# Kernel tuning notes

Measured on AMD Instinct MI355X. Metric: run time of the kernel, lower is better.

The kernel has to match this reference:

```python
import jax, jax.numpy as jnp
import numpy as np

N = 50000   # nodes
E = 800000  # edges per timestep
T = 2
IN_C = 128
HID = 128


def gcn_conv(x, src, dst, W, b):
    """PyG GCNConv: add self-loops, symmetric normalization, linear, scatter-add, bias."""
    n = x.shape[0]
    loop = jnp.arange(n, dtype=src.dtype)
    s = jnp.concatenate([src, loop])  # [E+N]
    d = jnp.concatenate([dst, loop])
    h = x @ W                          # [N, H]
    deg = jax.ops.segment_sum(jnp.ones_like(d, dtype=x.dtype), d, num_segments=n)
    dinv = jnp.where(deg > 0, jax.lax.rsqrt(deg), 0.0)
    norm = dinv[s] * dinv[d]           # [E+N]
    msg = h[s] * norm[:, None]         # gather + scale
    out = jax.ops.segment_sum(msg, d, num_segments=n)  # scatter-add
    return out + b


def setup_inputs() -> dict:
    key = jax.random.key(0)
    ks = jax.random.split(key, 6)
    x_seq = jax.random.normal(ks[0], (T, N, IN_C), dtype=jnp.float32)
    edge_indices = jax.random.randint(ks[1], (T, 2, E), 0, N, dtype=jnp.int64)
    W1 = jax.random.normal(ks[2], (IN_C, HID), dtype=jnp.float32) * (1.0 / np.sqrt(IN_C))
    b1 = jnp.zeros((HID,), dtype=jnp.float32)
    W2 = jax.random.normal(ks[3], (HID, HID), dtype=jnp.float32) * (1.0 / np.sqrt(HID))
    b2 = jnp.zeros((HID,), dtype=jnp.float32)
    Wc = jax.random.normal(ks[4], (HID, 1), dtype=jnp.float32) * (1.0 / np.sqrt(HID))
    bc = jnp.zeros((1,), dtype=jnp.float32)
    return {"x_seq": x_seq, "edge_indices": edge_indices, "W1": W1, "b1": b1,
            "W2": W2, "b2": b2, "Wc": Wc, "bc": bc}


def reference(x_seq, edge_indices, W1, b1, W2, b2, Wc, bc):
    outputs = []
    for t in range(T):  # small fixed timestep loop, as in original
        x_t = x_seq[t]
        src = edge_indices[t, 0]
        dst = edge_indices[t, 1]
        h = jax.nn.relu(gcn_conv(x_t, src, dst, W1, b1))
        # dropout is inference-identity (eval mode)
        h = gcn_conv(h, src, dst, W2, b2)
        outputs.append(h)
    final = outputs[-1]
    importance_out = (final @ Wc + bc).squeeze(-1)  # [N]
    return (importance_out, *outputs)
```

## Files before the change

kernel.cpp:

```cpp
#include <hip/hip_runtime.h>
#include <hip/hip_bf16.h>

typedef unsigned int u32;
typedef unsigned short u16;
typedef unsigned long long u64;
typedef __bf16 bf16x8 __attribute__((ext_vector_type(8)));
typedef short short8 __attribute__((ext_vector_type(8)));
typedef float floatx4 __attribute__((ext_vector_type(4)));

__device__ inline float b2f(u16 b) { return __uint_as_float((u32)b << 16); }
__device__ inline float lo2f(u32 p) { return __uint_as_float(p << 16); }
__device__ inline float hi2f(u32 p) { return __uint_as_float(p & 0xffff0000u); }
__device__ inline u16 f2bs(float f) {
    __hip_bfloat16 h = __float2bfloat16(f);
    return *reinterpret_cast<u16*>(&h);
}
__device__ inline float ldext(const void* p, int fl, int i) {
    return fl ? ((const float*)p)[i] : b2f(((const u16*)p)[i]);
}

__global__ __launch_bounds__(64) void detect_kernel(const int* __restrict__ eb,
                                                    const u32* __restrict__ xw,
                                                    int* __restrict__ flags,
                                                    int S, int n) {
    __shared__ int sh[64 * 3];
    int lane = threadIdx.x & 63;
    int zc = 0, explo = 0;
#pragma unroll
    for (int r = 0; r < 4; ++r) {
        int i = 64 * r + lane;
        zc += (eb[2 * i + 1] == 0) ? 1 : 0;
        u32 w = xw[i];
        int e = (int)((w >> 7) & 0xFF);
        explo += (e >= 96 && e <= 140) ? 1 : 0;
    }
    sh[lane] = zc;
    sh[64 + lane] = explo;
    __syncthreads();
    int fl = 0;
    {
        int z = 0;
        for (int j = 0; j < 64; ++j) z += sh[j];
        fl = (z > 200) ? 1 : 0;
    }
    int vc = 0;
#pragma unroll
    for (int r = 0; r < 4; ++r) {
        int li = S / 2 + 64 * r + lane;
        int v = fl ? eb[2 * li] : eb[li];
        vc += ((unsigned)v < (unsigned)n) ? 1 : 0;
    }
    sh[128 + lane] = vc;
    __syncthreads();
    if (lane == 0) {
        int vtot = 0, etot = 0;
        for (int j = 0; j < 64; ++j) vtot += sh[128 + j];
        for (int j = 0; j < 64; ++j) etot += sh[64 + j];
        flags[0] = fl;
        flags[1] = (etot >= 192) ? 0 : 1;
        flags[2] = (vtot >= 240) ? (S / 4) : (S / 8);
    }
}

__device__ inline int load_edge(const int* eb, int fl, int idx) {
    return eb[fl ? (idx << 1) : idx];
}

#define PCHUNK 4096
__global__ __launch_bounds__(256) void part_kernel(const int* __restrict__ eb,
                                                   const int* __restrict__ flags,
                                                   int* __restrict__ bkcnt,
                                                   u64* __restrict__ pairs,
                                                   int n, int shift, int capP) {
    __shared__ int cnt[512];
    __shared__ int gbase[512];
    const int E = flags[2];
    const int fl = flags[0];
    const int nbuk = (2 * n + (1 << shift) - 1) >> shift;
    const int tid = threadIdx.x;
    for (int i = tid; i < nbuk; i += 256) cnt[i] = 0;
    __syncthreads();
    const int e0 = blockIdx.x * PCHUNK;
    u32 sv[16]; int gv[16], rk[16];
#pragma unroll
    for (int j = 0; j < 16; ++j) {
        int e = e0 + j * 256 + tid;
        u32 gs = 0; int g = -1;
        if (e < 2 * E) {
            int t = (e >= E) ? 1 : 0;
            int le = e - t * E;
            gs = (u32)(t * n) + (u32)load_edge(eb, fl, t * 2 * E + le);
            unsigned du = (unsigned)load_edge(eb, fl, t * 2 * E + E + le);
            if (du < (unsigned)n) g = t * n + (int)du;
        }
        sv[j] = gs;
        gv[j] = g;
        rk[j] = (g >= 0) ? atomicAdd(&cnt[g >> shift], 1) : 0;
    }
    __syncthreads();
    for (int b = tid; b < nbuk; b += 256) {
        int c = cnt[b];
        gbase[b] = c ? atomicAdd(&bkcnt[b], c) : 0;
    }
    __syncthreads();
#pragma unroll
    for (int j = 0; j < 16; ++j) {
        if (gv[j] >= 0) {
            int b = gv[j] >> shift;
            int idx = gbase[b] + rk[j];
            if (idx < capP)
                pairs[(size_t)b * capP + idx] =
                    ((u64)(u32)gv[j] << 32) | sv[j];
        }
    }
}

__global__ __launch_bounds__(256) void scat_kernel(const u64* __restrict__ pairs,
                                                   const int* __restrict__ bkcnt,
                                                   int* __restrict__ deg,
                                                   int* __restrict__ off,
                                                   float* __restrict__ dinv,
                                                   int* __restrict__ ssrc,
                                                   int n2, int shift, int capP) {
    __shared__ int hist[1024];
    __shared__ int lscan[256];
    const int b = blockIdx.x;
    const int d0 = b << shift;
    if (d0 >= n2) return;
    int nn = (1 << shift);
    if (d0 + nn > n2) nn = n2 - d0;
    const int tid = threadIdx.x;
    for (int j = tid; j < nn; j += 256) hist[j] = 0;
    __syncthreads();
    int cnt = bkcnt[b];
    if (cnt > capP) cnt = capP;
    const int gb = b * capP;
    const u64* pb = pairs + (size_t)gb;
    for (int i = tid; i < cnt; i += 256) {
        unsigned dl = (unsigned)(int)(pb[i] >> 32) - (unsigned)d0;
        if (dl < (unsigned)nn) atomicAdd(&hist[dl], 1);
    }
    __syncthreads();
    int base4 = tid * 4;
    int s0 = 0, s1 = 0, s2 = 0, s3 = 0;
    if (base4 < nn) {
        s0 = hist[base4];
        s1 = (base4 + 1 < nn) ? hist[base4 + 1] : 0;
        s2 = (base4 + 2 < nn) ? hist[base4 + 2] : 0;
        s3 = (base4 + 3 < nn) ? hist[base4 + 3] : 0;
    }
    int p0 = (s0 + 3) & ~3, p1 = (s1 + 3) & ~3;
    int p2 = (s2 + 3) & ~3, p3 = (s3 + 3) & ~3;
    int tsum = p0 + p1 + p2 + p3;
    lscan[tid] = tsum;
    __syncthreads();
    int val = tsum;
    for (int o = 1; o < 256; o <<= 1) {
        int add = (tid >= o) ? lscan[tid - o] : 0;
        __syncthreads();
        val += add;
        lscan[tid] = val;
        __syncthreads();
    }
    int texcl = val - tsum;
    if (base4 < nn) {
        int g = d0 + base4;
        int o0 = gb + texcl;
        deg[g] = s0; off[g] = o0; dinv[g] = rsqrtf((float)(s0 + 1));
        hist[base4] = o0;
        if (base4 + 1 < nn) {
            int o1 = o0 + p0;
            deg[g + 1] = s1; off[g + 1] = o1; dinv[g + 1] = rsqrtf((float)(s1 + 1));
            hist[base4 + 1] = o1;
        }
        if (base4 + 2 < nn) {
            int o2 = o0 + p0 + p1;
            deg[g + 2] = s2; off[g + 2] = o2; dinv[g + 2] = rsqrtf((float)(s2 + 1));
            hist[base4 + 2] = o2;
        }
        if (base4 + 3 < nn) {
            int o3 = o0 + p0 + p1 + p2;
            deg[g + 3] = s3; off[g + 3] = o3; dinv[g + 3] = rsqrtf((float)(s3 + 1));
            hist[base4 + 3] = o3;
        }
    }
    __syncthreads();
    const int limit = gb + capP;
    for (int i = tid; i < cnt; i += 256) {
        u64 p = pb[i];
        unsigned dl = (unsigned)(int)(p >> 32) - (unsigned)d0;
        if (dl < (unsigned)nn) {
            int pos = atomicAdd(&hist[dl], 1);
            if (pos < limit) ssrc[pos] = (int)(u32)p;
        }
    }
}

__global__ __launch_bounds__(256) void prep_w(const void* __restrict__ W1,
                                              const void* __restrict__ W2,
                                              const int* __restrict__ flags,
                                              u16* __restrict__ W1t,
                                              u16* __restrict__ W2t) {
    int tid = blockIdx.x * 256 + threadIdx.x;
    if (tid < 2 * 128 * 128) {
        int which = tid >> 14;
        int r = tid & 16383;
        const void* W = which ? W2 : W1;
        u16* Wt = which ? W2t : W1t;
        int c = r >> 7, k = r & 127;
        Wt[c * 128 + k] = f2bs(ldext(W, flags[1], k * 128 + c));
    }
}

__global__ __launch_bounds__(256) void gemm_mfma(const void* __restrict__ Xv,
                                                 int x_ext,
                                                 const u16* __restrict__ Wt,
                                                 const int* __restrict__ flags,
                                                 const float* __restrict__ dinv,
                                                 u16* __restrict__ hs, int n) {
    __shared__ u16 Ws[128 * 136];
    {
        u32* wsu = (u32*)Ws;
        const u32* wtu = (const u32*)Wt;
        for (int i = threadIdx.x; i < 128 * 64; i += 256) {
            int c = i >> 6, kk = i & 63;
            wsu[c * 68 + kk] = wtu[i];
        }
    }
    __syncthreads();

    const int wave = threadIdx.x >> 6;
    const int lane = threadIdx.x & 63;
    const int m = lane & 15;
    const int quad = lane >> 4;
    const int node0 = blockIdx.x * 64 + wave * 16;
    if (node0 >= n) return;

    const int xf32 = x_ext ? flags[1] : 0;
    int va = node0 + m;
    if (va > n - 1) va = n - 1;

    floatx4 acc[8];
#pragma unroll
    for (int t = 0; t < 8; ++t) acc[t] = (floatx4){0.f, 0.f, 0.f, 0.f};

#pragma unroll
    for (int ks = 0; ks < 4; ++ks) {
        bf16x8 a;
        if (xf32) {
            const float* Xf = (const float*)Xv + (size_t)va * 128 + ks * 32 + quad * 8;
            float4 x0 = *(const float4*)Xf;
            float4 x1 = *(const float4*)(Xf + 4);
            short8 as;
            as[0] = (short)f2bs(x0.x); as[1] = (short)f2bs(x0.y);
            as[2] = (short)f2bs(x0.z); as[3] = (short)f2bs(x0.w);
            as[4] = (short)f2bs(x1.x); as[5] = (short)f2bs(x1.y);
            as[6] = (short)f2bs(x1.z); as[7] = (short)f2bs(x1.w);
            a = __builtin_bit_cast(bf16x8, as);
        } else {
            const u16* Xb = (const u16*)Xv + (size_t)va * 128 + ks * 32 + quad * 8;
            a = *(const bf16x8*)Xb;
        }
#pragma unroll
        for (int t = 0; t < 8; ++t) {
            const bf16x8 b = *(const bf16x8*)(Ws + (16 * t + m) * 136 + ks * 32 + quad * 8);
            acc[t] = __builtin_amdgcn_mfma_f32_16x16x32_bf16(a, b, acc[t], 0, 0, 0);
        }
    }

#pragma unroll
    for (int r = 0; r < 4; ++r) {
        int v = node0 + quad * 4 + r;
        if (v < n) {
            float dv = dinv[v];
#pragma unroll
            for (int t = 0; t < 8; ++t)
                hs[(size_t)v * 128 + 16 * t + m] = f2bs(acc[t][r] * dv);
        }
    }
}

__global__ __launch_bounds__(256) void gather_kernel(const u16* __restrict__ hs,
                                                     const int* __restrict__ off,
                                                     const int* __restrict__ deg,
                                                     const int* __restrict__ ssrc,
                                                     const float* __restrict__ dinv,
                                                     const void* __restrict__ bias,
                                                     const int* __restrict__ flags,
                                                     float* __restrict__ outf,
                                                     u16* __restrict__ outb,
                                                     const void* __restrict__ Wc,
                                                     const void* __restrict__ bc,
                                                     float* __restrict__ imp,
                                                     int n2, int half, int relu) {
    int w = (blockIdx.x * 256 + threadIdx.x) >> 6;
    int lane = threadIdx.x & 63;
    if (w >= n2) return;

    const u32* hsu = (const u32*)hs;
    const unsigned nm1 = (unsigned)(n2 - 1);
    const unsigned zrow = (unsigned)n2;

    u32 pself = hsu[(size_t)w * 64 + lane];
    float ax = lo2f(pself), ay = hi2f(pself);
    int i = __builtin_amdgcn_readfirstlane(off[w]);
    int end = i + __builtin_amdgcn_readfirstlane(deg[w]);

    float bx = 0.f, by = 0.f, cx = 0.f, cy = 0.f, dx = 0.f, dy = 0.f;

    for (; i + 16 <= end; i += 16) {
        int4 qa = *(const int4*)(ssrc + i);
        int4 qb = *(const int4*)(ssrc + i + 4);
        int4 qc = *(const int4*)(ssrc + i + 8);
        int4 qd = *(const int4*)(ssrc + i + 12);
        unsigned s0 = (unsigned)qa.x; if (s0 > nm1) s0 = zrow;
        unsigned s1 = (unsigned)qa.y; if (s1 > nm1) s1 = zrow;
        unsigned s2 = (unsigned)qa.z; if (s2 > nm1) s2 = zrow;
        unsigned s3 = (unsigned)qa.w; if (s3 > nm1) s3 = zrow;
        unsigned s4 = (unsigned)qb.x; if (s4 > nm1) s4 = zrow;
        unsigned s5 = (unsigned)qb.y; if (s5 > nm1) s5 = zrow;
        unsigned s6 = (unsigned)qb.z; if (s6 > nm1) s6 = zrow;
        unsigned s7 = (unsigned)qb.w; if (s7 > nm1) s7 = zrow;
        unsigned s8 = (unsigned)qc.x; if (s8 > nm1) s8 = zrow;
        unsigned s9 = (unsigned)qc.y; if (s9 > nm1) s9 = zrow;
        unsigned sa = (unsigned)qc.z; if (sa > nm1) sa = zrow;
        unsigned sb = (unsigned)qc.w; if (sb > nm1) sb = zrow;
        unsigned sc = (unsigned)qd.x; if (sc > nm1) sc = zrow;
        unsigned sd = (unsigned)qd.y; if (sd > nm1) sd = zrow;
        unsigned se = (unsigned)qd.z; if (se > nm1) se = zrow;
        unsigned sf = (unsigned)qd.w; if (sf > nm1) sf = zrow;
        u32 v0 = hsu[(size_t)s0 * 64 + lane];
        u32 v1 = hsu[(size_t)s1 * 64 + lane];
        u32 v2 = hsu[(size_t)s2 * 64 + lane];
        u32 v3 = hsu[(size_t)s3 * 64 + lane];
        u32 v4 = hsu[(size_t)s4 * 64 + lane];
        u32 v5 = hsu[(size_t)s5 * 64 + lane];
        u32 v6 = hsu[(size_t)s6 * 64 + lane];
        u32 v7 = hsu[(size_t)s7 * 64 + lane];
        u32 v8 = hsu[(size_t)s8 * 64 + lane];
        u32 v9 = hsu[(size_t)s9 * 64 + lane];
        u32 va = hsu[(size_t)sa * 64 + lane];
        u32 vb = hsu[(size_t)sb * 64 + lane];
        u32 vc = hsu[(size_t)sc * 64 + lane];
        u32 vd = hsu[(size_t)sd * 64 + lane];
        u32 ve = hsu[(size_t)se * 64 + lane];
        u32 vf = hsu[(size_t)sf * 64 + lane];
        ax += lo2f(v0); ay += hi2f(v0);
        bx += lo2f(v1); by += hi2f(v1);
        cx += lo2f(v2); cy += hi2f(v2);
        dx += lo2f(v3); dy += hi2f(v3);
        ax += lo2f(v4); ay += hi2f(v4);
        bx += lo2f(v5); by += hi2f(v5);
        cx += lo2f(v6); cy += hi2f(v6);
        dx += lo2f(v7); dy += hi2f(v7);
        ax += lo2f(v8); ay += hi2f(v8);
        bx += lo2f(v9); by += hi2f(v9);
        cx += lo2f(va); cy += hi2f(va);
        dx += lo2f(vb); dy += hi2f(vb);
        ax += lo2f(vc); ay += hi2f(vc);
        bx += lo2f(vd); by += hi2f(vd);
        cx += lo2f(ve); cy += hi2f(ve);
        dx += lo2f(vf); dy += hi2f(vf);
    }
    for (; i < end; i += 4) {
        int4 qa = *(const int4*)(ssrc + i);
        unsigned s0 = (unsigned)qa.x; if (s0 > nm1) s0 = zrow;
        unsigned s1 = (unsigned)qa.y; if (i + 1 >= end || s1 > nm1) s1 = zrow;
        unsigned s2 = (unsigned)qa.z; if (i + 2 >= end || s2 > nm1) s2 = zrow;
        unsigned s3 = (unsigned)qa.w; if (i + 3 >= end || s3 > nm1) s3 = zrow;
        u32 v0 = hsu[(size_t)s0 * 64 + lane];
        u32 v1 = hsu[(size_t)s1 * 64 + lane];
        u32 v2 = hsu[(size_t)s2 * 64 + lane];
        u32 v3 = hsu[(size_t)s3 * 64 + lane];
        ax += lo2f(v0); ay += hi2f(v0);
        bx += lo2f(v1); by += hi2f(v1);
        cx += lo2f(v2); cy += hi2f(v2);
        dx += lo2f(v3); dy += hi2f(v3);
    }
    ax += bx + cx + dx;
    ay += by + cy + dy;

    int ffl = flags[1];
    float dv = dinv[w];
    float o0 = dv * ax + ldext(bias, ffl, 2 * lane);
    float o1 = dv * ay + ldext(bias, ffl, 2 * lane + 1);
    if (relu) {
        o0 = fmaxf(o0, 0.f);
        o1 = fmaxf(o1, 0.f);
    }
    if (outf) ((float2*)outf)[(size_t)w * 64 + lane] = make_float2(o0, o1);
    else ((u32*)outb)[(size_t)w * 64 + lane] = (u32)f2bs(o0) | ((u32)f2bs(o1) << 16);

    if (imp && w >= half) {
        float cb = o0 * ldext(Wc, ffl, 2 * lane) + o1 * ldext(Wc, ffl, 2 * lane + 1);
        cb += __shfl_xor(cb, 32);
        cb += __shfl_xor(cb, 16);
        cb += __shfl_xor(cb, 8);
        cb += __shfl_xor(cb, 4);
        cb += __shfl_xor(cb, 2);
        cb += __shfl_xor(cb, 1);
        if (lane == 0) imp[w - half] = cb + ldext(bc, ffl, 0);
    }
}

extern "C" void kernel_launch(void* const* d_in, const int* in_sizes, int n_in,
                              void* d_out, int out_size, void* d_ws, size_t ws_size,
                              hipStream_t stream) {
    const int T = 2, C = 128;
    const int N = in_sizes[0] / (T * C);
    const int S = in_sizes[1];
    const int Emax = S / 4;
    const int N2 = 2 * N;

    const void* x_seq = d_in[0];
    const int* edges = (const int*)d_in[1];
    const void* W1 = d_in[2];
    const void* b1 = d_in[3];
    const void* W2 = d_in[4];
    const void* b2 = d_in[5];
    const void* Wc = d_in[6];
    const void* bc = d_in[7];

    float* out = (float*)d_out;
    float* R = out + N;

    char* p = (char*)d_ws;
    auto alloc = [&](size_t bytes) {
        char* r = p;
        p += (bytes + 255) & ~(size_t)255;
        return r;
    };
    int* flags = (int*)alloc(256);
    int* deg = (int*)alloc((size_t)N2 * 4);
    int* off = (int*)alloc((size_t)N2 * 4);
    float* dinv = (float*)alloc((size_t)N2 * 4);
    int* bkcnt = (int*)alloc(512 * 4);

    int shift = 8;
    while ((((N2 + (1 << shift) - 1) >> shift) > 512) && shift < 10) ++shift;
    const int NBUK = (N2 + (1 << shift) - 1) >> shift;
    const size_t aliasBytes = (size_t)2 * N2 * C * 2;
    const int capP = (int)(aliasBytes / (8 * (size_t)NBUK)) & ~3;

    int* ssrc = (int*)alloc(((size_t)NBUK * capP + 256) * 4);
    u16* W1t = (u16*)alloc(128 * 128 * 2);
    u16* W2t = (u16*)alloc(128 * 128 * 2);
    u16* hsb = (u16*)alloc((size_t)(N2 + 2) * C * 2);
    u16* hmb = (u16*)alloc((size_t)N2 * C * 2);
    u64* pairs = (u64*)hsb;

    const int gP = (2 * Emax + PCHUNK - 1) / PCHUNK;
    const int gN2 = (N2 + 3) / 4;
    const int gG2 = (N2 + 63) / 64;
    const int gW = (2 * 128 * 128 + 255) / 256;

    detect_kernel<<<1, 64, 0, stream>>>(edges, (const u32*)x_seq, flags, S, N);
    prep_w<<<gW, 256, 0, stream>>>(W1, W2, flags, W1t, W2t);

    hipMemsetAsync(bkcnt, 0, 512 * 4, stream);
    part_kernel<<<gP, 256, 0, stream>>>(edges, flags, bkcnt, pairs, N, shift, capP);
    scat_kernel<<<NBUK, 256, 0, stream>>>(pairs, bkcnt, deg, off, dinv,
                                          ssrc, N2, shift, capP);
    hipMemsetAsync(hsb + (size_t)N2 * C, 0, C * 2, stream);

    gemm_mfma<<<gG2, 256, 0, stream>>>(x_seq, 1, W1t, flags, dinv, hsb, N2);
    gather_kernel<<<gN2, 256, 0, stream>>>(hsb, off, deg, ssrc, dinv, b1, flags,
                                           (float*)nullptr, hmb,
                                           nullptr, nullptr, (float*)nullptr,
                                           N2, N, 1);

    gemm_mfma<<<gG2, 256, 0, stream>>>(hmb, 0, W2t, flags, dinv, hsb, N2);
    gather_kernel<<<gN2, 256, 0, stream>>>(hsb, off, deg, ssrc, dinv, b2, flags,
                                           R, (u16*)nullptr,
                                           Wc, bc, out,
                                           N2, N, 0);
}
```

Before: 291.5 us.

## Fold memsets and weight prep into other kernels; persistent grid-stride gather

Zeroing of the bucket counters moves into detect_kernel and zeroing of the padding row moves into gemm_mfma, which removes two memset calls. The weight transpose is appended as extra blocks of part_kernel, removing the separate prep_w launch. The gather kernel becomes a persistent grid-stride loop over 2048 blocks that prefetches the next node's offset and degree and hoists the bias loads out of the loop. The aim is to cut launch and tail overhead, at the cost of less parallelism per node and some ordering risk for the padding row write.

```diff
diff --git a/kernel.cpp b/kernel.cpp
--- a/kernel.cpp
+++ b/kernel.cpp
@@ -22,9 +22,11 @@
 __global__ __launch_bounds__(64) void detect_kernel(const int* __restrict__ eb,
                                                     const u32* __restrict__ xw,
                                                     int* __restrict__ flags,
+                                                    int* __restrict__ bkcnt,
                                                     int S, int n) {
     __shared__ int sh[64 * 3];
     int lane = threadIdx.x & 63;
+    for (int j = lane; j < 512; j += 64) bkcnt[j] = 0;
     int zc = 0, explo = 0;
 #pragma unroll
     for (int r = 0; r < 4; ++r) {
@@ -71,9 +73,26 @@
                                                    const int* __restrict__ flags,
                                                    int* __restrict__ bkcnt,
                                                    u64* __restrict__ pairs,
-                                                   int n, int shift, int capP) {
+                                                   int n, int shift, int capP,
+                                                   int gP,
+                                                   const void* __restrict__ W1,
+                                                   const void* __restrict__ W2,
+                                                   u16* __restrict__ W1t,
+                                                   u16* __restrict__ W2t) {
     __shared__ int cnt[512];
     __shared__ int gbase[512];
+    if ((int)blockIdx.x >= gP) {
+        int tid = (blockIdx.x - gP) * 256 + threadIdx.x;
+        if (tid < 2 * 128 * 128) {
+            int which = tid >> 14;
+            int r = tid & 16383;
+            const void* W = which ? W2 : W1;
+            u16* Wt = which ? W2t : W1t;
+            int c = r >> 7, k = r & 127;
+            Wt[c * 128 + k] = f2bs(ldext(W, flags[1], k * 128 + c));
+        }
+        return;
+    }
     const int E = flags[2];
     const int fl = flags[0];
     const int nbuk = (2 * n + (1 << shift) - 1) >> shift;
@@ -196,28 +215,14 @@
     }
 }
 
-__global__ __launch_bounds__(256) void prep_w(const void* __restrict__ W1,
-                                              const void* __restrict__ W2,
-                                              const int* __restrict__ flags,
-                                              u16* __restrict__ W1t,
-                                              u16* __restrict__ W2t) {
-    int tid = blockIdx.x * 256 + threadIdx.x;
-    if (tid < 2 * 128 * 128) {
-        int which = tid >> 14;
-        int r = tid & 16383;
-        const void* W = which ? W2 : W1;
-        u16* Wt = which ? W2t : W1t;
-        int c = r >> 7, k = r & 127;
-        Wt[c * 128 + k] = f2bs(ldext(W, flags[1], k * 128 + c));
-    }
-}
-
 __global__ __launch_bounds__(256) void gemm_mfma(const void* __restrict__ Xv,
                                                  int x_ext,
                                                  const u16* __restrict__ Wt,
                                                  const int* __restrict__ flags,
                                                  const float* __restrict__ dinv,
                                                  u16* __restrict__ hs, int n) {
+    if (blockIdx.x == 0 && threadIdx.x < 64)
+        ((u32*)hs)[(size_t)n * 64 + threadIdx.x] = 0;
     __shared__ u16 Ws[128 * 136];
     {
         u32* wsu = (u32*)Ws;
@@ -292,114 +297,130 @@
                                                      const void* __restrict__ Wc,
                                                      const void* __restrict__ bc,
                                                      float* __restrict__ imp,
-                                                     int n2, int half, int relu) {
+                                                     int n2, int half, int relu,
+                                                     int nwaves) {
+    const int lane = threadIdx.x & 63;
     int w = (blockIdx.x * 256 + threadIdx.x) >> 6;
-    int lane = threadIdx.x & 63;
     if (w >= n2) return;
 
     const u32* hsu = (const u32*)hs;
     const unsigned nm1 = (unsigned)(n2 - 1);
     const unsigned zrow = (unsigned)n2;
-
-    u32 pself = hsu[(size_t)w * 64 + lane];
-    float ax = lo2f(pself), ay = hi2f(pself);
-    int i = __builtin_amdgcn_readfirstlane(off[w]);
-    int end = i + __builtin_amdgcn_readfirstlane(deg[w]);
-
-    float bx = 0.f, by = 0.f, cx = 0.f, cy = 0.f, dx = 0.f, dy = 0.f;
-
-    for (; i + 16 <= end; i += 16) {
-        int4 qa = *(const int4*)(ssrc + i);
-        int4 qb = *(const int4*)(ssrc + i + 4);
-        int4 qc = *(const int4*)(ssrc + i + 8);
-        int4 qd = *(const int4*)(ssrc + i + 12);
-        unsigned s0 = (unsigned)qa.x; if (s0 > nm1) s0 = zrow;
-        unsigned s1 = (unsigned)qa.y; if (s1 > nm1) s1 = zrow;
-        unsigned s2 = (unsigned)qa.z; if (s2 > nm1) s2 = zrow;
-        unsigned s3 = (unsigned)qa.w; if (s3 > nm1) s3 = zrow;
-        unsigned s4 = (unsigned)qb.x; if (s4 > nm1) s4 = zrow;
-        unsigned s5 = (unsigned)qb.y; if (s5 > nm1) s5 = zrow;
-        unsigned s6 = (unsigned)qb.z; if (s6 > nm1) s6 = zrow;
-        unsigned s7 = (unsigned)qb.w; if (s7 > nm1) s7 = zrow;
-        unsigned s8 = (unsigned)qc.x; if (s8 > nm1) s8 = zrow;
-        unsigned s9 = (unsigned)qc.y; if (s9 > nm1) s9 = zrow;
-        unsigned sa = (unsigned)qc.z; if (sa > nm1) sa = zrow;
-        unsigned sb = (unsigned)qc.w; if (sb > nm1) sb = zrow;
-        unsigned sc = (unsigned)qd.x; if (sc > nm1) sc = zrow;
-        unsigned sd = (unsigned)qd.y; if (sd > nm1) sd = zrow;
-        unsigned se = (unsigned)qd.z; if (se > nm1) se = zrow;
-        unsigned sf = (unsigned)qd.w; if (sf > nm1) sf = zrow;
-        u32 v0 = hsu[(size_t)s0 * 64 + lane];
-        u32 v1 = hsu[(size_t)s1 * 64 + lane];
-        u32 v2 = hsu[(size_t)s2 * 64 + lane];
-        u32 v3 = hsu[(size_t)s3 * 64 + lane];
-        u32 v4 = hsu[(size_t)s4 * 64 + lane];
-        u32 v5 = hsu[(size_t)s5 * 64 + lane];
-        u32 v6 = hsu[(size_t)s6 * 64 + lane];
-        u32 v7 = hsu[(size_t)s7 * 64 + lane];
-        u32 v8 = hsu[(size_t)s8 * 64 + lane];
-        u32 v9 = hsu[(size_t)s9 * 64 + lane];
-        u32 va = hsu[(size_t)sa * 64 + lane];
-        u32 vb = hsu[(size_t)sb * 64 + lane];
-        u32 vc = hsu[(size_t)sc * 64 + lane];
-        u32 vd = hsu[(size_t)sd * 64 + lane];
-        u32 ve = hsu[(size_t)se * 64 + lane];
-        u32 vf = hsu[(size_t)sf * 64 + lane];
-        ax += lo2f(v0); ay += hi2f(v0);
-        bx += lo2f(v1); by += hi2f(v1);
-        cx += lo2f(v2); cy += hi2f(v2);
-        dx += lo2f(v3); dy += hi2f(v3);
-        ax += lo2f(v4); ay += hi2f(v4);
-        bx += lo2f(v5); by += hi2f(v5);
-        cx += lo2f(v6); cy += hi2f(v6);
-        dx += lo2f(v7); dy += hi2f(v7);
-        ax += lo2f(v8); ay += hi2f(v8);
-        bx += lo2f(v9); by += hi2f(v9);
-        cx += lo2f(va); cy += hi2f(va);
-        dx += lo2f(vb); dy += hi2f(vb);
-        ax += lo2f(vc); ay += hi2f(vc);
-        bx += lo2f(vd); by += hi2f(vd);
-        cx += lo2f(ve); cy += hi2f(ve);
-        dx += lo2f(vf); dy += hi2f(vf);
-    }
-    for (; i < end; i += 4) {
-        int4 qa = *(const int4*)(ssrc + i);
-        unsigned s0 = (unsigned)qa.x; if (s0 > nm1) s0 = zrow;
-        unsigned s1 = (unsigned)qa.y; if (i + 1 >= end || s1 > nm1) s1 = zrow;
-        unsigned s2 = (unsigned)qa.z; if (i + 2 >= end || s2 > nm1) s2 = zrow;
-        unsigned s3 = (unsigned)qa.w; if (i + 3 >= end || s3 > nm1) s3 = zrow;
-        u32 v0 = hsu[(size_t)s0 * 64 + lane];
-        u32 v1 = hsu[(size_t)s1 * 64 + lane];
-        u32 v2 = hsu[(size_t)s2 * 64 + lane];
-        u32 v3 = hsu[(size_t)s3 * 64 + lane];
-        ax += lo2f(v0); ay += hi2f(v0);
-        bx += lo2f(v1); by += hi2f(v1);
-        cx += lo2f(v2); cy += hi2f(v2);
-        dx += lo2f(v3); dy += hi2f(v3);
-    }
-    ax += bx + cx + dx;
-    ay += by + cy + dy;
-
-    int ffl = flags[1];
-    float dv = dinv[w];
-    float o0 = dv * ax + ldext(bias, ffl, 2 * lane);
-    float o1 = dv * ay + ldext(bias, ffl, 2 * lane + 1);
-    if (relu) {
-        o0 = fmaxf(o0, 0.f);
-        o1 = fmaxf(o1, 0.f);
-    }
-    if (outf) ((float2*)outf)[(size_t)w * 64 + lane] = make_float2(o0, o1);
-    else ((u32*)outb)[(size_t)w * 64 + lane] = (u32)f2bs(o0) | ((u32)f2bs(o1) << 16);
-
-    if (imp && w >= half) {
-        float cb = o0 * ldext(Wc, ffl, 2 * lane) + o1 * ldext(Wc, ffl, 2 * lane + 1);
-        cb += __shfl_xor(cb, 32);
-        cb += __shfl_xor(cb, 16);
-        cb += __shfl_xor(cb, 8);
-        cb += __shfl_xor(cb, 4);
-        cb += __shfl_xor(cb, 2);
-        cb += __shfl_xor(cb, 1);
-        if (lane == 0) imp[w - half] = cb + ldext(bc, ffl, 0);
+    const int ffl = flags[1];
+    const float bias0 = ldext(bias, ffl, 2 * lane);
+    const float bias1 = ldext(bias, ffl, 2 * lane + 1);
+
+    int curOff = off[w];
+    int curDeg = deg[w];
+
+    while (w < n2) {
+        const int wn = w + nwaves;
+        int nOff = 0, nDeg = 0;
+        if (wn < n2) { nOff = off[wn]; nDeg = deg[wn]; }
+
+        u32 pself = hsu[(size_t)w * 64 + lane];
+        float ax = lo2f(pself), ay = hi2f(pself);
+        int i = __builtin_amdgcn_readfirstlane(curOff);
+        int end = i + __builtin_amdgcn_readfirstlane(curDeg);
+
+        float bx = 0.f, by = 0.f, cx = 0.f, cy = 0.f, dx = 0.f, dy = 0.f;
+
+        for (; i + 16 <= end; i += 16) {
+            int4 qa = *(const int4*)(ssrc + i);
+            int4 qb = *(const int4*)(ssrc + i + 4);
+            int4 qc = *(const int4*)(ssrc + i + 8);
+            int4 qd = *(const int4*)(ssrc + i + 12);
+            unsigned s0 = (unsigned)qa.x; if (s0 > nm1) s0 = zrow;
+            unsigned s1 = (unsigned)qa.y; if (s1 > nm1) s1 = zrow;
+            unsigned s2 = (unsigned)qa.z; if (s2 > nm1) s2 = zrow;
+            unsigned s3 = (unsigned)qa.w; if (s3 > nm1) s3 = zrow;
+            unsigned s4 = (unsigned)qb.x; if (s4 > nm1) s4 = zrow;
+            unsigned s5 = (unsigned)qb.y; if (s5 > nm1) s5 = zrow;
+            unsigned s6 = (unsigned)qb.z; if (s6 > nm1) s6 = zrow;
+            unsigned s7 = (unsigned)qb.w; if (s7 > nm1) s7 = zrow;
+            unsigned s8 = (unsigned)qc.x; if (s8 > nm1) s8 = zrow;
+            unsigned s9 = (unsigned)qc.y; if (s9 > nm1) s9 = zrow;
+            unsigned sa = (unsigned)qc.z; if (sa > nm1) sa = zrow;
+            unsigned sb = (unsigned)qc.w; if (sb > nm1) sb = zrow;
+            unsigned sc = (unsigned)qd.x; if (sc > nm1) sc = zrow;
+            unsigned sd = (unsigned)qd.y; if (sd > nm1) sd = zrow;
+            unsigned se = (unsigned)qd.z; if (se > nm1) se = zrow;
+            unsigned sf = (unsigned)qd.w; if (sf > nm1) sf = zrow;
+            u32 v0 = hsu[(size_t)s0 * 64 + lane];
+            u32 v1 = hsu[(size_t)s1 * 64 + lane];
+            u32 v2 = hsu[(size_t)s2 * 64 + lane];
+            u32 v3 = hsu[(size_t)s3 * 64 + lane];
+            u32 v4 = hsu[(size_t)s4 * 64 + lane];
+            u32 v5 = hsu[(size_t)s5 * 64 + lane];
+            u32 v6 = hsu[(size_t)s6 * 64 + lane];
+            u32 v7 = hsu[(size_t)s7 * 64 + lane];
+            u32 v8 = hsu[(size_t)s8 * 64 + lane];
+            u32 v9 = hsu[(size_t)s9 * 64 + lane];
+            u32 va = hsu[(size_t)sa * 64 + lane];
+            u32 vb = hsu[(size_t)sb * 64 + lane];
+            u32 vc = hsu[(size_t)sc * 64 + lane];
+            u32 vd = hsu[(size_t)sd * 64 + lane];
+            u32 ve = hsu[(size_t)se * 64 + lane];
+            u32 vf = hsu[(size_t)sf * 64 + lane];
+            ax += lo2f(v0); ay += hi2f(v0);
+            bx += lo2f(v1); by += hi2f(v1);
+            cx += lo2f(v2); cy += hi2f(v2);
+            dx += lo2f(v3); dy += hi2f(v3);
+            ax += lo2f(v4); ay += hi2f(v4);
+            bx += lo2f(v5); by += hi2f(v5);
+            cx += lo2f(v6); cy += hi2f(v6);
+            dx += lo2f(v7); dy += hi2f(v7);
+            ax += lo2f(v8); ay += hi2f(v8);
+            bx += lo2f(v9); by += hi2f(v9);
+            cx += lo2f(va); cy += hi2f(va);
+            dx += lo2f(vb); dy += hi2f(vb);
+            ax += lo2f(vc); ay += hi2f(vc);
+            bx += lo2f(vd); by += hi2f(vd);
+            cx += lo2f(ve); cy += hi2f(ve);
+            dx += lo2f(vf); dy += hi2f(vf);
+        }
+        for (; i < end; i += 4) {
+            int4 qa = *(const int4*)(ssrc + i);
+            unsigned s0 = (unsigned)qa.x; if (s0 > nm1) s0 = zrow;
+            unsigned s1 = (unsigned)qa.y; if (i + 1 >= end || s1 > nm1) s1 = zrow;
+            unsigned s2 = (unsigned)qa.z; if (i + 2 >= end || s2 > nm1) s2 = zrow;
+            unsigned s3 = (unsigned)qa.w; if (i + 3 >= end || s3 > nm1) s3 = zrow;
+            u32 v0 = hsu[(size_t)s0 * 64 + lane];
+            u32 v1 = hsu[(size_t)s1 * 64 + lane];
+            u32 v2 = hsu[(size_t)s2 * 64 + lane];
+            u32 v3 = hsu[(size_t)s3 * 64 + lane];
+            ax += lo2f(v0); ay += hi2f(v0);
+            bx += lo2f(v1); by += hi2f(v1);
+            cx += lo2f(v2); cy += hi2f(v2);
+            dx += lo2f(v3); dy += hi2f(v3);
+        }
+        ax += bx + cx + dx;
+        ay += by + cy + dy;
+
+        float dv = dinv[w];
+        float o0 = dv * ax + bias0;
+        float o1 = dv * ay + bias1;
+        if (relu) {
+            o0 = fmaxf(o0, 0.f);
+            o1 = fmaxf(o1, 0.f);
+        }
+        if (outf) ((float2*)outf)[(size_t)w * 64 + lane] = make_float2(o0, o1);
+        else ((u32*)outb)[(size_t)w * 64 + lane] = (u32)f2bs(o0) | ((u32)f2bs(o1) << 16);
+
+        if (imp && w >= half) {
+            float cb = o0 * ldext(Wc, ffl, 2 * lane) + o1 * ldext(Wc, ffl, 2 * lane + 1);
+            cb += __shfl_xor(cb, 32);
+            cb += __shfl_xor(cb, 16);
+            cb += __shfl_xor(cb, 8);
+            cb += __shfl_xor(cb, 4);
+            cb += __shfl_xor(cb, 2);
+            cb += __shfl_xor(cb, 1);
+            if (lane == 0) imp[w - half] = cb + ldext(bc, ffl, 0);
+        }
+
+        w = wn;
+        curOff = nOff;
+        curDeg = nDeg;
     }
 }
 
@@ -450,28 +471,27 @@
     u64* pairs = (u64*)hsb;
 
     const int gP = (2 * Emax + PCHUNK - 1) / PCHUNK;
-    const int gN2 = (N2 + 3) / 4;
+    const int gW = (2 * 128 * 128 + 255) / 256;
+    const int gGA = 2048;
+    const int nwaves = gGA * 4;
     const int gG2 = (N2 + 63) / 64;
-    const int gW = (2 * 128 * 128 + 255) / 256;
-
-    detect_kernel<<<1, 64, 0, stream>>>(edges, (const u32*)x_seq, flags, S, N);
-    prep_w<<<gW, 256, 0, stream>>>(W1, W2, flags, W1t, W2t);
-
-    hipMemsetAsync(bkcnt, 0, 512 * 4, stream);
-    part_kernel<<<gP, 256, 0, stream>>>(edges, flags, bkcnt, pairs, N, shift, capP);
+
+    detect_kernel<<<1, 64, 0, stream>>>(edges, (const u32*)x_seq, flags, bkcnt, S, N);
+
+    part_kernel<<<gP + gW, 256, 0, stream>>>(edges, flags, bkcnt, pairs, N, shift,
+                                             capP, gP, W1, W2, W1t, W2t);
     scat_kernel<<<NBUK, 256, 0, stream>>>(pairs, bkcnt, deg, off, dinv,
                                           ssrc, N2, shift, capP);
-    hipMemsetAsync(hsb + (size_t)N2 * C, 0, C * 2, stream);
 
     gemm_mfma<<<gG2, 256, 0, stream>>>(x_seq, 1, W1t, flags, dinv, hsb, N2);
-    gather_kernel<<<gN2, 256, 0, stream>>>(hsb, off, deg, ssrc, dinv, b1, flags,
+    gather_kernel<<<gGA, 256, 0, stream>>>(hsb, off, deg, ssrc, dinv, b1, flags,
                                            (float*)nullptr, hmb,
                                            nullptr, nullptr, (float*)nullptr,
-                                           N2, N, 1);
+                                           N2, N, 1, nwaves);
 
     gemm_mfma<<<gG2, 256, 0, stream>>>(hmb, 0, W2t, flags, dinv, hsb, N2);
-    gather_kernel<<<gN2, 256, 0, stream>>>(hsb, off, deg, ssrc, dinv, b2, flags,
+    gather_kernel<<<gGA, 256, 0, stream>>>(hsb, off, deg, ssrc, dinv, b2, flags,
                                            R, (u16*)nullptr,
                                            Wc, bc, out,
-                                           N2, N, 0);
-}
+                                           N2, N, 0, nwaves);
+}
```

New measurement: 327.1 us. +12.2%, slower.
